# Optimization experiments

Hardware: AMD Instinct MI355X
Metric: run time of the kernel (lower is better)

## Reference

```python
import jax, jax.numpy as jnp
import numpy as np

N = 20000      # total atoms
M = 12         # neighbors per atom
B = 41         # nbr_fea_len
ORIG = 92      # orig_atom_fea_len
F = 64         # atom_fea_len
D = 2 * F + B  # 169, gated feature width
NC = 3         # n_conv
K = 3          # k parallel gates per conv
H = 128        # h_fea_len
N0 = 400       # crystals in batch
EPS = 1e-5     # batchnorm eps


def setup_inputs() -> dict:
    key = jax.random.key(0)
    ks = jax.random.split(key, 24)
    inp = {}
    inp["atom_fea"] = jax.random.normal(ks[0], (N, ORIG), jnp.float32)
    inp["nbr_fea"] = jax.random.normal(ks[1], (N, M, B), jnp.float32)
    inp["nbr_fea_idx"] = jax.random.randint(ks[2], (N, M), 0, N)
    inp["crystal_atom_idx"] = jnp.sort(jax.random.randint(ks[3], (N,), 0, N0))
    inp["n_crystals"] = N0
    inp["emb_w"] = jax.random.normal(ks[4], (ORIG, F)) * 0.1
    inp["emb_b"] = jnp.zeros((F,), jnp.float32)
    inp["fc_w"] = jax.random.normal(ks[5], (NC, K, D, D)) * 0.05
    inp["fc_b"] = jnp.zeros((NC, K, D), jnp.float32)
    inp["bn1_g"] = jnp.ones((NC, K, D), jnp.float32)
    inp["bn1_b"] = jnp.zeros((NC, K, D), jnp.float32)
    inp["bn1_m"] = jax.random.normal(ks[6], (NC, K, D)) * 0.1
    inp["bn1_v"] = jax.random.uniform(ks[7], (NC, K, D)) * 0.5 + 0.75
    inp["bn2_g"] = jnp.ones((NC, K, F), jnp.float32)
    inp["bn2_b"] = jnp.zeros((NC, K, F), jnp.float32)
    inp["bn2_m"] = jax.random.normal(ks[8], (NC, K, F)) * 0.1
    inp["bn2_v"] = jax.random.uniform(ks[9], (NC, K, F)) * 0.5 + 0.75
    inp["atom_w"] = jax.random.normal(ks[10], (NC, K, 2 * K)) * 0.3
    inp["atom_b"] = jnp.zeros((NC, 2 * K), jnp.float32)
    inp["nbr_w"] = jax.random.normal(ks[11], (NC, K, 2 * K)) * 0.3
    inp["nbr_b"] = jnp.zeros((NC, 2 * K), jnp.float32)
    inp["fc1_w"] = jax.random.normal(ks[12], (F, H)) * 0.1
    inp["fc1_b"] = jnp.zeros((H,), jnp.float32)
    inp["out_w"] = jax.random.normal(ks[13], (H, 1)) * 0.1
    inp["out_b"] = jnp.zeros((1,), jnp.float32)
    return inp


def _conv(atom_in, nbr, idx, fc_w, fc_b, bn1_g, bn1_b, bn1_m, bn1_v,
          bn2_g, bn2_b, bn2_m, bn2_v, atom_w, atom_b, nbr_w, nbr_b):
    n, m = idx.shape
    gathered = atom_in[idx]                                   # (N,M,F) irregular gather
    self_f = jnp.broadcast_to(atom_in[:, None, :], (n, m, F))
    total = jnp.concatenate([self_f, gathered, nbr], axis=2)  # (N,M,D)
    # k parallel linear layers, vectorized over k
    g = jnp.einsum('nmd,kde->knme', total, fc_w) + fc_b[:, None, None, :]  # (K,N,M,D)
    # bn1 (eval mode, running stats)
    g = (g - bn1_m[:, None, None, :]) * jax.lax.rsqrt(bn1_v[:, None, None, :] + EPS) \
        * bn1_g[:, None, None, :] + bn1_b[:, None, None, :]
    nbr_filter = jax.nn.softmax(g[..., :F], axis=2)            # softmax over neighbors M
    nbr_core = jax.nn.relu(g[..., F:2 * F])
    new_nbr_k = g[..., 2 * F:] + nbr[None]                     # (K,N,M,B) residual on bonds
    summed = jnp.sum(nbr_filter * nbr_core, axis=2)            # (K,N,F)
    summed = (summed - bn2_m[:, None, :]) * jax.lax.rsqrt(bn2_v[:, None, :] + EPS) \
        * bn2_g[:, None, :] + bn2_b[:, None, :]
    out_k = atom_in[None] + summed                             # (K,N,F) residual on atoms
    out = jnp.moveaxis(out_k, 0, 2)                            # (N,F,K)
    new_nbr = jnp.moveaxis(new_nbr_k, 0, 3)                    # (N,M,B,K)
    og = out @ atom_w + atom_b                                 # (N,F,2K)
    ng = new_nbr @ nbr_w + nbr_b                               # (N,M,B,2K)
    out = jnp.sum(og[..., :K] * jax.nn.softmax(og[..., K:], axis=2), axis=2)
    new_nbr = jnp.sum(ng[..., :K] * jax.nn.softmax(ng[..., K:], axis=3), axis=3)
    return out, new_nbr


def reference(atom_fea, nbr_fea, nbr_fea_idx, crystal_atom_idx, n_crystals,
              emb_w, emb_b, fc_w, fc_b, bn1_g, bn1_b, bn1_m, bn1_v,
              bn2_g, bn2_b, bn2_m, bn2_v, atom_w, atom_b, nbr_w, nbr_b,
              fc1_w, fc1_b, out_w, out_b):
    x = atom_fea @ emb_w + emb_b                               # embedding
    nbr = nbr_fea
    for i in range(NC):                                        # fixed small layer loop
        x, nbr = _conv(x, nbr, nbr_fea_idx,
                       fc_w[i], fc_b[i], bn1_g[i], bn1_b[i], bn1_m[i], bn1_v[i],
                       bn2_g[i], bn2_b[i], bn2_m[i], bn2_v[i],
                       atom_w[i], atom_b[i], nbr_w[i], nbr_b[i])
    # per-crystal mean pooling via segment sum
    sums = jax.ops.segment_sum(x, crystal_atom_idx, num_segments=n_crystals)
    counts = jax.ops.segment_sum(jnp.ones((x.shape[0], 1), x.dtype),
                                 crystal_atom_idx, num_segments=n_crystals)
    crys = sums / jnp.maximum(counts, 1.0)
    crys = jax.nn.relu(crys) @ fc1_w + fc1_b
    crys = jax.nn.relu(crys)
    return crys @ out_w + out_b                                # (N0, 1)
```

## Files before the change

kernel.cpp:

```cpp
#include <hip/hip_runtime.h>
#include <math.h>

#define N_ATOMS 20000
#define M 12
#define B 41
#define ORIG 92
#define F 64
#define D 169
#define NCONV 3
#define K 3
#define TWOK 6
#define H 128
#define N0 400
#define EPS 1e-5f
#define KB (K * B)
#define NBRS 42

#define KPAD 192
#define NS 6
#define ATOMS_PER_BLK 4
#define ROWS (ATOMS_PER_BLK * 16)
#define THREADS 512
#define LFRAG 98304
#define WT_USHORTS (NCONV * 2 * LFRAG)
#define GRID (N_ATOMS / ATOMS_PER_BLK)

typedef __attribute__((ext_vector_type(8))) short bf16x8;
typedef __attribute__((ext_vector_type(4))) float f32x4;

__device__ inline unsigned short f32_to_bf16(float v) {
    unsigned int x = __float_as_uint(v);
    unsigned int r = (x + 0x7fffu + ((x >> 16) & 1u)) >> 16;
    return (unsigned short)r;
}
__device__ inline float bf16_to_f32(unsigned short u) {
    return __uint_as_float(((unsigned int)u) << 16);
}
__device__ inline unsigned int pack_hilo(float v) {
    unsigned short hi = f32_to_bf16(v);
    unsigned short lo = f32_to_bf16(v - bf16_to_f32(hi));
    return (unsigned int)hi | ((unsigned int)lo << 16);
}
__device__ inline float unpack_hilo(unsigned int p) {
    return bf16_to_f32((unsigned short)(p & 0xFFFFu)) +
           bf16_to_f32((unsigned short)(p >> 16));
}

__global__ void emb_kernel(const float* __restrict__ atom_fea,
                           const float* __restrict__ emb_w,
                           const float* __restrict__ emb_b,
                           float* __restrict__ x,
                           unsigned int* __restrict__ xp) {
    int i = blockIdx.x * blockDim.x + threadIdx.x;
    if (i >= N_ATOMS * F) return;
    int n = i / F, f = i % F;
    const float* a = atom_fea + n * ORIG;
    float acc = emb_b[f];
    #pragma unroll 4
    for (int d = 0; d < ORIG; ++d)
        acc = fmaf(a[d], emb_w[d * F + f], acc);
    x[i] = acc;
    xp[i] = pack_hilo(acc);
}

__global__ void npack_kernel(const float* __restrict__ nbr_fea,
                             unsigned int* __restrict__ nbrp) {
    int i = blockIdx.x * blockDim.x + threadIdx.x;
    if (i >= N_ATOMS * M * NBRS) return;
    int nm = i / NBRS, slot = i - nm * NBRS;
    nbrp[i] = (slot < B) ? pack_hilo(nbr_fea[nm * B + slot]) : 0u;
}

__global__ void prep_kernel(const float* __restrict__ fc_w,
                            unsigned short* __restrict__ wt) {
    int i = blockIdx.x * blockDim.x + threadIdx.x;
    if (i >= NCONV * LFRAG) return;
    int layer = i / LFRAG;
    int r = i % LFRAG;
    int s = r / 16384;
    int r2 = r % 16384;
    int c16 = r2 / 512;
    int r3 = r2 % 512;
    int lane = r3 / 8;
    int e = r3 % 8;
    int col = c16 * 16 + (lane & 15);
    int k = s * 32 + (lane >> 4) * 8 + e;
    float v = 0.f;
    if (k < D) {
        int b3 = col >> 7, cc = col & 127;
        if (b3 < 3) {
            v = fc_w[((size_t)(layer * K + b3) * D + k) * D + cc];
        } else if (cc < KB) {
            int kk = cc / B, bb = cc - kk * B;
            v = fc_w[((size_t)(layer * K + kk) * D + k) * D + 2 * F + bb];
        }
    }
    unsigned short hi = f32_to_bf16(v);
    float hf = bf16_to_f32(hi);
    unsigned short lo = f32_to_bf16(v - hf);
    size_t off = (size_t)s * 16384 + c16 * 512 + lane * 8 + e;
    wt[(size_t)(layer * 2 + 0) * LFRAG + off] = hi;
    wt[(size_t)(layer * 2 + 1) * LFRAG + off] = lo;
}

__global__ void prep2_kernel(const float* __restrict__ fc_b,
                             const float* __restrict__ bn1_g,
                             const float* __restrict__ bn1_b,
                             const float* __restrict__ bn1_m,
                             const float* __restrict__ bn1_v,
                             const float* __restrict__ bn2_g,
                             const float* __restrict__ bn2_b,
                             const float* __restrict__ bn2_m,
                             const float* __restrict__ bn2_v,
                             float* __restrict__ sc1,
                             float* __restrict__ sh1,
                             float* __restrict__ sc2,
                             float* __restrict__ sh2) {
    int i = blockIdx.x * blockDim.x + threadIdx.x;
    if (i < NCONV * K * D) {
        float sc = bn1_g[i] * rsqrtf(bn1_v[i] + EPS);
        sc1[i] = sc;
        sh1[i] = fmaf(fc_b[i], sc, bn1_b[i] - bn1_m[i] * sc);
    }
    if (i < NCONV * K * F) {
        float sc = bn2_g[i] * rsqrtf(bn2_v[i] + EPS);
        sc2[i] = sc;
        sh2[i] = bn2_b[i] - bn2_m[i] * sc;
    }
}

template <bool NEED_NBR>
__global__ __launch_bounds__(THREADS, 4)
void conv_mfma(const float* __restrict__ xin,
               const unsigned int* __restrict__ xpin,
               const unsigned int* __restrict__ nbrpin,
               const int* __restrict__ idx,
               const unsigned short* __restrict__ wtl,
               const float* __restrict__ sc1,
               const float* __restrict__ sh1,
               const float* __restrict__ sc2,
               const float* __restrict__ sh2,
               const float* __restrict__ atom_w,
               const float* __restrict__ atom_b,
               const float* __restrict__ nbr_w,
               const float* __restrict__ nbr_b,
               float* __restrict__ xout,
               unsigned int* __restrict__ xpout,
               unsigned int* __restrict__ nbrpout) {
    __shared__ unsigned short s_a[2 * ROWS * KPAD];
    __shared__ float s_sum[ATOMS_PER_BLK * K * F];

    const int t = threadIdx.x;
    const int w = t >> 6;
    const int l = t & 63;
    const int l15 = l & 15;
    const int lane3 = l >> 4;
    const int n0 = blockIdx.x * ATOMS_PER_BLK;

    {
        const int srow = t >> 3;
        const int j8 = t & 7;
        const int a = srow >> 4, m = srow & 15;
        const int n = n0 + a;
        const unsigned int mask = (unsigned int)((srow & 7) << 4);
        char* hi_base = (char*)s_a + srow * (KPAD * 2);
        char* lo_base = hi_base + 2 * ROWS * KPAD;
        if (m < M) {
            const unsigned int* xs = xpin + n * F;
            const unsigned int* xg = xpin + idx[n * M + m] * F;
            const unsigned int* nb = nbrpin + (size_t)(n * M + m) * NBRS;
            #pragma unroll
            for (int q = 0; q < 12; ++q) {
                int kp = j8 + 8 * q;
                uint2 u;
                if (kp < 32)       u = *(const uint2*)&xs[kp * 2];
                else if (kp < 64)  u = *(const uint2*)&xg[kp * 2 - 64];
                else if (kp < 85)  u = *(const uint2*)&nb[kp * 2 - 128];
                else               u = make_uint2(0u, 0u);
                unsigned int hip = (u.x & 0xFFFFu) | (u.y << 16);
                unsigned int lop = (u.x >> 16) | (u.y & 0xFFFF0000u);
                unsigned int byo = ((unsigned int)(kp * 4)) ^ mask;
                *(unsigned int*)(hi_base + byo) = hip;
                *(unsigned int*)(lo_base + byo) = lop;
            }
        } else {
            #pragma unroll
            for (int q = 0; q < 12; ++q) {
                unsigned int byo = ((unsigned int)((j8 + 8 * q) * 4)) ^ mask;
                *(unsigned int*)(hi_base + byo) = 0u;
                *(unsigned int*)(lo_base + byo) = 0u;
            }
        }
    }
    __syncthreads();

    const int kk_gate = w >> 1, half = w & 1;
    int tile[4];
    if (w < 6) {
        tile[0] = kk_gate * 8 + half * 2 + 0;
        tile[1] = kk_gate * 8 + half * 2 + 1;
        tile[2] = tile[0] + 4;
        tile[3] = tile[1] + 4;
    } else {
        tile[0] = 24 + (w - 6) * 4 + 0;
        tile[1] = 24 + (w - 6) * 4 + 1;
        tile[2] = 24 + (w - 6) * 4 + 2;
        tile[3] = 24 + (w - 6) * 4 + 3;
    }

    f32x4 acc[ATOMS_PER_BLK][4];
    #pragma unroll
    for (int a = 0; a < ATOMS_PER_BLK; ++a)
        #pragma unroll
        for (int j = 0; j < 4; ++j)
            acc[a][j] = (f32x4){0.f, 0.f, 0.f, 0.f};

    if (!(w >= 6 && !NEED_NBR)) {
        for (int s = 0; s < NS; ++s) {
            bf16x8 ah[ATOMS_PER_BLK], al[ATOMS_PER_BLK];
            #pragma unroll
            for (int a = 0; a < ATOMS_PER_BLK; ++a) {
                int row = a * 16 + l15;
                int koff = s * 64 + lane3 * 16;
                int byte = row * (KPAD * 2) + (koff ^ ((row & 7) << 4));
                ah[a] = *reinterpret_cast<const bf16x8*>(&s_a[byte >> 1]);
                al[a] = *reinterpret_cast<const bf16x8*>(&s_a[(byte >> 1) + ROWS * KPAD]);
            }
            #pragma unroll
            for (int j = 0; j < 4; ++j) {
                const unsigned short* wp =
                    wtl + (size_t)s * 16384 + tile[j] * 512 + l * 8;
                bf16x8 bh = *reinterpret_cast<const bf16x8*>(wp);
                bf16x8 bl = *reinterpret_cast<const bf16x8*>(wp + LFRAG);
                #pragma unroll
                for (int a = 0; a < ATOMS_PER_BLK; ++a) {
                    acc[a][j] = __builtin_amdgcn_mfma_f32_16x16x32_bf16(ah[a], bh, acc[a][j], 0, 0, 0);
                    acc[a][j] = __builtin_amdgcn_mfma_f32_16x16x32_bf16(ah[a], bl, acc[a][j], 0, 0, 0);
                    acc[a][j] = __builtin_amdgcn_mfma_f32_16x16x32_bf16(al[a], bh, acc[a][j], 0, 0, 0);
                }
            }
        }
    }
    __syncthreads();

    float* s_nnk = reinterpret_cast<float*>(s_a);

    if (w < 6) {
        const int k = kk_gate;
        #pragma unroll
        for (int a = 0; a < ATOMS_PER_BLK; ++a) {
            #pragma unroll
            for (int j = 0; j < 2; ++j) {
                int e = (half * 2 + j) * 16 + l15;
                int cf = k * D + e, cr = cf + F, c2 = k * F + e;
                float sc_f = sc1[cf], sh_f = sh1[cf];
                float sc_c = sc1[cr], sh_c = sh1[cr];
                bool act = (lane3 < 3);
                float fv[4], cv[4];
                #pragma unroll
                for (int r = 0; r < 4; ++r) {
                    fv[r] = fmaf(acc[a][j][r], sc_f, sh_f);
                    cv[r] = fmaxf(fmaf(acc[a][j + 2][r], sc_c, sh_c), 0.f);
                }
                float mx = act ? fmaxf(fmaxf(fv[0], fv[1]), fmaxf(fv[2], fv[3])) : -1e30f;
                mx = fmaxf(mx, __shfl_xor(mx, 16));
                mx = fmaxf(mx, __shfl_xor(mx, 32));
                float se = 0.f, sp = 0.f;
                #pragma unroll
                for (int r = 0; r < 4; ++r) {
                    float ex = act ? __expf(fv[r] - mx) : 0.f;
                    se += ex;
                    sp = fmaf(ex, cv[r], sp);
                }
                se += __shfl_xor(se, 16);
                se += __shfl_xor(se, 32);
                sp += __shfl_xor(sp, 16);
                sp += __shfl_xor(sp, 32);
                float summed = sp / se;
                float outv = xin[(n0 + a) * F + e] + fmaf(summed, sc2[c2], sh2[c2]);
                if (lane3 == 0) s_sum[(a * K + k) * F + e] = outv;
            }
        }
    } else if (NEED_NBR) {
        #pragma unroll
        for (int a = 0; a < ATOMS_PER_BLK; ++a) {
            #pragma unroll
            for (int j = 0; j < 4; ++j) {
                int cc = (w - 6) * 64 + j * 16 + l15;
                if (cc < KB) {
                    int kk = cc / B, bb = cc - (cc / B) * B;
                    int col = kk * D + 2 * F + bb;
                    float sc = sc1[col], sh = sh1[col];
                    #pragma unroll
                    for (int r = 0; r < 4; ++r) {
                        int m = lane3 * 4 + r;
                        if (m < M) {
                            float nv = unpack_hilo(
                                nbrpin[(size_t)((n0 + a) * M + m) * NBRS + bb]);
                            s_nnk[((a * K + kk) * M + m) * B + bb] =
                                fmaf(acc[a][j][r], sc, sh) + nv;
                        }
                    }
                }
            }
        }
    }
    __syncthreads();

    if (t < ATOMS_PER_BLK * F) {
        int a2 = t >> 6, f = t & 63;
        float og[TWOK];
        #pragma unroll
        for (int j = 0; j < TWOK; ++j) {
            float v = atom_b[j];
            #pragma unroll
            for (int q = 0; q < K; ++q)
                v = fmaf(s_sum[(a2 * K + q) * F + f], atom_w[q * TWOK + j], v);
            og[j] = v;
        }
        float mx = fmaxf(fmaxf(og[K], og[K + 1]), og[K + 2]);
        float e0 = __expf(og[K] - mx), e1 = __expf(og[K + 1] - mx), e2 = __expf(og[K + 2] - mx);
        float inv = 1.f / (e0 + e1 + e2);
        float outv = (og[0] * e0 + og[1] * e1 + og[2] * e2) * inv;
        xout[(n0 + a2) * F + f] = outv;
        xpout[(n0 + a2) * F + f] = pack_hilo(outv);
    }

    if (NEED_NBR) {
        for (int i = t; i < ATOMS_PER_BLK * M * B; i += THREADS) {
            int a2 = i / (M * B);
            int r = i - a2 * (M * B);
            int m = r / B, b = r - m * B;
            float ng[TWOK];
            #pragma unroll
            for (int j = 0; j < TWOK; ++j) {
                float v = nbr_b[j];
                #pragma unroll
                for (int q = 0; q < K; ++q)
                    v = fmaf(s_nnk[((a2 * K + q) * M + m) * B + b], nbr_w[q * TWOK + j], v);
                ng[j] = v;
            }
            float mx = fmaxf(fmaxf(ng[K], ng[K + 1]), ng[K + 2]);
            float e0 = __expf(ng[K] - mx), e1 = __expf(ng[K + 1] - mx), e2 = __expf(ng[K + 2] - mx);
            float inv = 1.f / (e0 + e1 + e2);
            float v = (ng[0] * e0 + ng[1] * e1 + ng[2] * e2) * inv;
            nbrpout[(size_t)((n0 + a2) * M + m) * NBRS + b] = pack_hilo(v);
        }
        for (int i3 = t; i3 < ATOMS_PER_BLK * M; i3 += THREADS) {
            int a2 = i3 / M, m = i3 - a2 * M;
            nbrpout[(size_t)((n0 + a2) * M + m) * NBRS + B] = 0u;
        }
    }
}

__global__ void pool_kernel(const float* __restrict__ x,
                            const int* __restrict__ cidx,
                            float* __restrict__ sums,
                            float* __restrict__ cnt) {
    int i = blockIdx.x * blockDim.x + threadIdx.x;
    if (i >= N_ATOMS * F) return;
    int n = i / F, f = i % F;
    int c = cidx[n];
    atomicAdd(&sums[c * F + f], x[i]);
    if (f == 0) atomicAdd(&cnt[c], 1.0f);
}

__global__ void head_kernel(const float* __restrict__ sums,
                            const float* __restrict__ cnt,
                            const float* __restrict__ fc1_w,
                            const float* __restrict__ fc1_b,
                            const float* __restrict__ out_w,
                            const float* __restrict__ out_b,
                            float* __restrict__ out) {
    const int c = blockIdx.x;
    const int t = threadIdx.x;
    __shared__ float a[F];
    __shared__ float red[H];
    float inv_cnt = 1.f / fmaxf(cnt[c], 1.0f);
    if (t < F) a[t] = fmaxf(sums[c * F + t] * inv_cnt, 0.f);
    __syncthreads();
    float hv = fc1_b[t];
    #pragma unroll 4
    for (int f = 0; f < F; ++f)
        hv = fmaf(a[f], fc1_w[f * H + t], hv);
    hv = fmaxf(hv, 0.f);
    red[t] = hv * out_w[t];
    __syncthreads();
    for (int s = H / 2; s > 0; s >>= 1) {
        if (t < s) red[t] += red[t + s];
        __syncthreads();
    }
    if (t == 0) out[c] = red[0] + out_b[0];
}

extern "C" void kernel_launch(void* const* d_in, const int* in_sizes, int n_in,
                              void* d_out, int out_size, void* d_ws, size_t ws_size,
                              hipStream_t stream) {
    (void)in_sizes; (void)n_in; (void)out_size; (void)ws_size;
    const float* atom_fea = (const float*)d_in[0];
    const float* nbr_fea  = (const float*)d_in[1];
    const int*   nbr_idx  = (const int*)d_in[2];
    const int*   cidx     = (const int*)d_in[3];
    const float* emb_w = (const float*)d_in[5];
    const float* emb_b = (const float*)d_in[6];
    const float* fc_w  = (const float*)d_in[7];
    const float* fc_b  = (const float*)d_in[8];
    const float* bn1_g = (const float*)d_in[9];
    const float* bn1_b = (const float*)d_in[10];
    const float* bn1_m = (const float*)d_in[11];
    const float* bn1_v = (const float*)d_in[12];
    const float* bn2_g = (const float*)d_in[13];
    const float* bn2_b = (const float*)d_in[14];
    const float* bn2_m = (const float*)d_in[15];
    const float* bn2_v = (const float*)d_in[16];
    const float* atom_w = (const float*)d_in[17];
    const float* atom_b = (const float*)d_in[18];
    const float* nbr_w  = (const float*)d_in[19];
    const float* nbr_b  = (const float*)d_in[20];
    const float* fc1_w  = (const float*)d_in[21];
    const float* fc1_b  = (const float*)d_in[22];
    const float* out_w  = (const float*)d_in[23];
    const float* out_b  = (const float*)d_in[24];
    float* out = (float*)d_out;

    float* xA   = (float*)d_ws;
    float* xB   = xA + (size_t)N_ATOMS * F;
    unsigned int* xPA = (unsigned int*)(xB + (size_t)N_ATOMS * F);
    unsigned int* xPB = xPA + (size_t)N_ATOMS * F;
    unsigned int* nbrP0 = xPB + (size_t)N_ATOMS * F;
    unsigned int* nbrPA = nbrP0 + (size_t)N_ATOMS * M * NBRS;
    float* sums = (float*)(nbrPA + (size_t)N_ATOMS * M * NBRS);
    float* cnt  = sums + (size_t)N0 * F;
    float* sc1  = cnt + N0;
    float* sh1  = sc1 + NCONV * K * D;
    float* sc2  = sh1 + NCONV * K * D;
    float* sh2  = sc2 + NCONV * K * F;
    unsigned short* wt = (unsigned short*)(sh2 + NCONV * K * F);

    prep_kernel<<<(NCONV * LFRAG + 255) / 256, 256, 0, stream>>>(fc_w, wt);
    prep2_kernel<<<(NCONV * K * D + 255) / 256, 256, 0, stream>>>(
        fc_b, bn1_g, bn1_b, bn1_m, bn1_v, bn2_g, bn2_b, bn2_m, bn2_v,
        sc1, sh1, sc2, sh2);
    npack_kernel<<<(N_ATOMS * M * NBRS + 255) / 256, 256, 0, stream>>>(nbr_fea, nbrP0);
    emb_kernel<<<(N_ATOMS * F + 255) / 256, 256, 0, stream>>>(
        atom_fea, emb_w, emb_b, xA, xPA);

    conv_mfma<true><<<GRID, THREADS, 0, stream>>>(
        xA, xPA, nbrP0, nbr_idx,
        wt, sc1, sh1, sc2, sh2,
        atom_w, atom_b, nbr_w, nbr_b, xB, xPB, nbrPA);
    conv_mfma<true><<<GRID, THREADS, 0, stream>>>(
        xB, xPB, nbrPA, nbr_idx,
        wt + (size_t)2 * LFRAG,
        sc1 + (size_t)1 * K * D, sh1 + (size_t)1 * K * D,
        sc2 + (size_t)1 * K * F, sh2 + (size_t)1 * K * F,
        atom_w + (size_t)1 * K * TWOK, atom_b + (size_t)1 * TWOK,
        nbr_w + (size_t)1 * K * TWOK, nbr_b + (size_t)1 * TWOK, xA, xPA, nbrP0);
    conv_mfma<false><<<GRID, THREADS, 0, stream>>>(
        xA, xPA, nbrP0, nbr_idx,
        wt + (size_t)4 * LFRAG,
        sc1 + (size_t)2 * K * D, sh1 + (size_t)2 * K * D,
        sc2 + (size_t)2 * K * F, sh2 + (size_t)2 * K * F,
        atom_w + (size_t)2 * K * TWOK, atom_b + (size_t)2 * TWOK,
        nbr_w + (size_t)2 * K * TWOK, nbr_b + (size_t)2 * TWOK, xB, xPB, nbrPA);

    hipMemsetAsync(sums, 0, (size_t)(N0 * F + N0) * sizeof(float), stream);
    pool_kernel<<<(N_ATOMS * F + 255) / 256, 256, 0, stream>>>(xB, cidx, sums, cnt);
    head_kernel<<<N0, H, 0, stream>>>(sums, cnt, fc1_w, fc1_b, out_w, out_b, out);
}
```

Baseline: 617.4 us.

## Precompute per-atom self/neighbor projections once, shrink per-edge GEMM to bond features

The gated linear layer is split by input block. The self-atom and neighbor-atom parts of the weight matrix are applied once per atom in a new pq_kernel, which writes a wide per-atom P/Q buffer. The per-edge MFMA then covers only the 41 bond features (one 64-wide K slab instead of 192). The edge kernel adds P for its own atom and gathers Q rows for each neighbor before batch norm, and it updates the packed bond buffer in place instead of ping-ponging. This removes the repeated per-edge matmul over atom features, but it adds a large intermediate buffer write per layer and scattered scalar reads of Q from global memory.

```diff
diff --git a/kernel.cpp b/kernel.cpp
--- a/kernel.cpp
+++ b/kernel.cpp
@@ -16,13 +16,12 @@
 #define KB (K * B)
 #define NBRS 42
 
-#define KPAD 192
-#define NS 6
+#define PQW 1024
+#define LFRAG_PQ 65536
+#define LFRAG_BD 32768
 #define ATOMS_PER_BLK 4
-#define ROWS (ATOMS_PER_BLK * 16)
+#define ROWS 64
 #define THREADS 512
-#define LFRAG 98304
-#define WT_USHORTS (NCONV * 2 * LFRAG)
 #define GRID (N_ATOMS / ATOMS_PER_BLK)
 
 typedef __attribute__((ext_vector_type(8))) short bf16x8;
@@ -44,6 +43,17 @@
 __device__ inline float unpack_hilo(unsigned int p) {
     return bf16_to_f32((unsigned short)(p & 0xFFFFu)) +
            bf16_to_f32((unsigned short)(p >> 16));
+}
+
+__device__ inline float wlookup(const float* __restrict__ fc_w,
+                                int layer, int row, int c) {
+    int b3 = c >> 7, cc = c & 127;
+    if (b3 < 3) return fc_w[((size_t)(layer * K + b3) * D + row) * D + cc];
+    if (cc < KB) {
+        int kk = cc / B, bb = cc - kk * B;
+        return fc_w[((size_t)(layer * K + kk) * D + row) * D + 2 * F + bb];
+    }
+    return 0.f;
 }
 
 __global__ void emb_kernel(const float* __restrict__ atom_fea,
@@ -71,36 +81,45 @@
     nbrp[i] = (slot < B) ? pack_hilo(nbr_fea[nm * B + slot]) : 0u;
 }
 
-__global__ void prep_kernel(const float* __restrict__ fc_w,
-                            unsigned short* __restrict__ wt) {
+__global__ void prep_pq_kernel(const float* __restrict__ fc_w,
+                               unsigned short* __restrict__ wtpq) {
     int i = blockIdx.x * blockDim.x + threadIdx.x;
-    if (i >= NCONV * LFRAG) return;
-    int layer = i / LFRAG;
-    int r = i % LFRAG;
+    if (i >= NCONV * LFRAG_PQ) return;
+    int layer = i / LFRAG_PQ;
+    int r = i % LFRAG_PQ;
+    int s = r / 32768;
+    int r2 = r % 32768;
+    int c16 = r2 / 512;
+    int r3 = r2 % 512;
+    int lane = r3 / 8, e = r3 % 8;
+    int isQ = (c16 >= 32);
+    int c = (isQ ? c16 - 32 : c16) * 16 + (lane & 15);
+    int row = (isQ ? F : 0) + s * 32 + (lane >> 4) * 8 + e;
+    float v = wlookup(fc_w, layer, row, c);
+    unsigned short hi = f32_to_bf16(v);
+    unsigned short lo = f32_to_bf16(v - bf16_to_f32(hi));
+    wtpq[(size_t)(layer * 2 + 0) * LFRAG_PQ + r] = hi;
+    wtpq[(size_t)(layer * 2 + 1) * LFRAG_PQ + r] = lo;
+}
+
+__global__ void prep_bond_kernel(const float* __restrict__ fc_w,
+                                 unsigned short* __restrict__ wtb) {
+    int i = blockIdx.x * blockDim.x + threadIdx.x;
+    if (i >= NCONV * LFRAG_BD) return;
+    int layer = i / LFRAG_BD;
+    int r = i % LFRAG_BD;
     int s = r / 16384;
     int r2 = r % 16384;
     int c16 = r2 / 512;
     int r3 = r2 % 512;
-    int lane = r3 / 8;
-    int e = r3 % 8;
-    int col = c16 * 16 + (lane & 15);
-    int k = s * 32 + (lane >> 4) * 8 + e;
-    float v = 0.f;
-    if (k < D) {
-        int b3 = col >> 7, cc = col & 127;
-        if (b3 < 3) {
-            v = fc_w[((size_t)(layer * K + b3) * D + k) * D + cc];
-        } else if (cc < KB) {
-            int kk = cc / B, bb = cc - kk * B;
-            v = fc_w[((size_t)(layer * K + kk) * D + k) * D + 2 * F + bb];
-        }
-    }
+    int lane = r3 / 8, e = r3 % 8;
+    int c = c16 * 16 + (lane & 15);
+    int row = 2 * F + s * 32 + (lane >> 4) * 8 + e;
+    float v = (row < D) ? wlookup(fc_w, layer, row, c) : 0.f;
     unsigned short hi = f32_to_bf16(v);
-    float hf = bf16_to_f32(hi);
-    unsigned short lo = f32_to_bf16(v - hf);
-    size_t off = (size_t)s * 16384 + c16 * 512 + lane * 8 + e;
-    wt[(size_t)(layer * 2 + 0) * LFRAG + off] = hi;
-    wt[(size_t)(layer * 2 + 1) * LFRAG + off] = lo;
+    unsigned short lo = f32_to_bf16(v - bf16_to_f32(hi));
+    wtb[(size_t)(layer * 2 + 0) * LFRAG_BD + r] = hi;
+    wtb[(size_t)(layer * 2 + 1) * LFRAG_BD + r] = lo;
 }
 
 __global__ void prep2_kernel(const float* __restrict__ fc_b,
@@ -129,13 +148,85 @@
     }
 }
 
+__global__ __launch_bounds__(512, 4)
+void pq_kernel(const unsigned int* __restrict__ xp,
+               const unsigned short* __restrict__ wtl,
+               float* __restrict__ pq) {
+    __shared__ __align__(16) unsigned short s_a[2 * 32 * 64];
+
+    const int t = threadIdx.x;
+    const int w = t >> 6, l = t & 63;
+    const int l15 = l & 15, lane3 = l >> 4;
+    const int n0 = blockIdx.x * 32;
+
+    {
+        int row = t >> 4, j16 = t & 15;
+        unsigned int mask = (unsigned int)((row & 7) << 4);
+        char* hb = (char*)s_a + row * 128;
+        const unsigned int* xr = xp + (n0 + row) * F;
+        #pragma unroll
+        for (int q = 0; q < 2; ++q) {
+            int kp = j16 + 16 * q;
+            uint2 u = *(const uint2*)&xr[kp * 2];
+            unsigned int hip = (u.x & 0xFFFFu) | (u.y << 16);
+            unsigned int lop = (u.x >> 16) | (u.y & 0xFFFF0000u);
+            unsigned int byo = ((unsigned int)(kp * 4)) ^ mask;
+            *(unsigned int*)(hb + byo) = hip;
+            *(unsigned int*)(hb + byo + 4096) = lop;
+        }
+    }
+    __syncthreads();
+
+    f32x4 acc[2][8];
+    #pragma unroll
+    for (int a = 0; a < 2; ++a)
+        #pragma unroll
+        for (int tt = 0; tt < 8; ++tt)
+            acc[a][tt] = (f32x4){0.f, 0.f, 0.f, 0.f};
+
+    #pragma unroll
+    for (int s = 0; s < 2; ++s) {
+        bf16x8 ah[2], al[2];
+        #pragma unroll
+        for (int a = 0; a < 2; ++a) {
+            int row = a * 16 + l15;
+            int byte = row * 128 + ((s * 64 + lane3 * 16) ^ ((row & 7) << 4));
+            ah[a] = *(const bf16x8*)((const char*)s_a + byte);
+            al[a] = *(const bf16x8*)((const char*)s_a + byte + 4096);
+        }
+        #pragma unroll
+        for (int tt = 0; tt < 8; ++tt) {
+            const unsigned short* wp = wtl + s * 32768 + (w * 8 + tt) * 512 + l * 8;
+            bf16x8 bh = *(const bf16x8*)wp;
+            bf16x8 bl = *(const bf16x8*)(wp + LFRAG_PQ);
+            #pragma unroll
+            for (int a = 0; a < 2; ++a) {
+                acc[a][tt] = __builtin_amdgcn_mfma_f32_16x16x32_bf16(ah[a], bh, acc[a][tt], 0, 0, 0);
+                acc[a][tt] = __builtin_amdgcn_mfma_f32_16x16x32_bf16(ah[a], bl, acc[a][tt], 0, 0, 0);
+                acc[a][tt] = __builtin_amdgcn_mfma_f32_16x16x32_bf16(al[a], bh, acc[a][tt], 0, 0, 0);
+            }
+        }
+    }
+
+    #pragma unroll
+    for (int a = 0; a < 2; ++a)
+        #pragma unroll
+        for (int tt = 0; tt < 8; ++tt) {
+            int col = (w * 8 + tt) * 16 + l15;
+            int rowb = n0 + a * 16 + lane3 * 4;
+            #pragma unroll
+            for (int r = 0; r < 4; ++r)
+                pq[(size_t)(rowb + r) * PQW + col] = acc[a][tt][r];
+        }
+}
+
 template <bool NEED_NBR>
 __global__ __launch_bounds__(THREADS, 4)
 void conv_mfma(const float* __restrict__ xin,
-               const unsigned int* __restrict__ xpin,
-               const unsigned int* __restrict__ nbrpin,
+               unsigned int* __restrict__ nbrp,
                const int* __restrict__ idx,
                const unsigned short* __restrict__ wtl,
+               const float* __restrict__ pq,
                const float* __restrict__ sc1,
                const float* __restrict__ sh1,
                const float* __restrict__ sc2,
@@ -145,50 +236,42 @@
                const float* __restrict__ nbr_w,
                const float* __restrict__ nbr_b,
                float* __restrict__ xout,
-               unsigned int* __restrict__ xpout,
-               unsigned int* __restrict__ nbrpout) {
-    __shared__ unsigned short s_a[2 * ROWS * KPAD];
+               unsigned int* __restrict__ xpout) {
+    __shared__ __align__(16) char s_mem[24576];
     __shared__ float s_sum[ATOMS_PER_BLK * K * F];
+    __shared__ int s_idx[ATOMS_PER_BLK * M];
 
     const int t = threadIdx.x;
-    const int w = t >> 6;
-    const int l = t & 63;
-    const int l15 = l & 15;
-    const int lane3 = l >> 4;
+    const int w = t >> 6, l = t & 63;
+    const int l15 = l & 15, lane3 = l >> 4;
     const int n0 = blockIdx.x * ATOMS_PER_BLK;
 
+    if (t < ATOMS_PER_BLK * M) s_idx[t] = idx[n0 * M + t];
+
     {
-        const int srow = t >> 3;
-        const int j8 = t & 7;
-        const int a = srow >> 4, m = srow & 15;
-        const int n = n0 + a;
-        const unsigned int mask = (unsigned int)((srow & 7) << 4);
-        char* hi_base = (char*)s_a + srow * (KPAD * 2);
-        char* lo_base = hi_base + 2 * ROWS * KPAD;
+        int srow = t >> 3, j8 = t & 7;
+        int a = srow >> 4, m = srow & 15;
+        unsigned int mask = (unsigned int)((srow & 7) << 4);
+        char* hb = s_mem + srow * 128;
         if (m < M) {
-            const unsigned int* xs = xpin + n * F;
-            const unsigned int* xg = xpin + idx[n * M + m] * F;
-            const unsigned int* nb = nbrpin + (size_t)(n * M + m) * NBRS;
-            #pragma unroll
-            for (int q = 0; q < 12; ++q) {
+            const unsigned int* nb = nbrp + (size_t)((n0 + a) * M + m) * NBRS;
+            #pragma unroll
+            for (int q = 0; q < 4; ++q) {
                 int kp = j8 + 8 * q;
-                uint2 u;
-                if (kp < 32)       u = *(const uint2*)&xs[kp * 2];
-                else if (kp < 64)  u = *(const uint2*)&xg[kp * 2 - 64];
-                else if (kp < 85)  u = *(const uint2*)&nb[kp * 2 - 128];
-                else               u = make_uint2(0u, 0u);
+                uint2 u = (kp < 21) ? *(const uint2*)&nb[kp * 2]
+                                    : make_uint2(0u, 0u);
                 unsigned int hip = (u.x & 0xFFFFu) | (u.y << 16);
                 unsigned int lop = (u.x >> 16) | (u.y & 0xFFFF0000u);
                 unsigned int byo = ((unsigned int)(kp * 4)) ^ mask;
-                *(unsigned int*)(hi_base + byo) = hip;
-                *(unsigned int*)(lo_base + byo) = lop;
+                *(unsigned int*)(hb + byo) = hip;
+                *(unsigned int*)(hb + byo + 8192) = lop;
             }
         } else {
             #pragma unroll
-            for (int q = 0; q < 12; ++q) {
+            for (int q = 0; q < 4; ++q) {
                 unsigned int byo = ((unsigned int)((j8 + 8 * q) * 4)) ^ mask;
-                *(unsigned int*)(hi_base + byo) = 0u;
-                *(unsigned int*)(lo_base + byo) = 0u;
+                *(unsigned int*)(hb + byo) = 0u;
+                *(unsigned int*)(hb + byo + 8192) = 0u;
             }
         }
     }
@@ -216,22 +299,21 @@
             acc[a][j] = (f32x4){0.f, 0.f, 0.f, 0.f};
 
     if (!(w >= 6 && !NEED_NBR)) {
-        for (int s = 0; s < NS; ++s) {
+        #pragma unroll
+        for (int s = 0; s < 2; ++s) {
             bf16x8 ah[ATOMS_PER_BLK], al[ATOMS_PER_BLK];
             #pragma unroll
             for (int a = 0; a < ATOMS_PER_BLK; ++a) {
                 int row = a * 16 + l15;
-                int koff = s * 64 + lane3 * 16;
-                int byte = row * (KPAD * 2) + (koff ^ ((row & 7) << 4));
-                ah[a] = *reinterpret_cast<const bf16x8*>(&s_a[byte >> 1]);
-                al[a] = *reinterpret_cast<const bf16x8*>(&s_a[(byte >> 1) + ROWS * KPAD]);
+                int byte = row * 128 + ((s * 64 + lane3 * 16) ^ ((row & 7) << 4));
+                ah[a] = *(const bf16x8*)(s_mem + byte);
+                al[a] = *(const bf16x8*)(s_mem + byte + 8192);
             }
             #pragma unroll
             for (int j = 0; j < 4; ++j) {
-                const unsigned short* wp =
-                    wtl + (size_t)s * 16384 + tile[j] * 512 + l * 8;
-                bf16x8 bh = *reinterpret_cast<const bf16x8*>(wp);
-                bf16x8 bl = *reinterpret_cast<const bf16x8*>(wp + LFRAG);
+                const unsigned short* wp = wtl + s * 16384 + tile[j] * 512 + l * 8;
+                bf16x8 bh = *(const bf16x8*)wp;
+                bf16x8 bl = *(const bf16x8*)(wp + LFRAG_BD);
                 #pragma unroll
                 for (int a = 0; a < ATOMS_PER_BLK; ++a) {
                     acc[a][j] = __builtin_amdgcn_mfma_f32_16x16x32_bf16(ah[a], bh, acc[a][j], 0, 0, 0);
@@ -243,24 +325,32 @@
     }
     __syncthreads();
 
-    float* s_nnk = reinterpret_cast<float*>(s_a);
+    float* s_nnk = (float*)s_mem;
 
     if (w < 6) {
         const int k = kk_gate;
         #pragma unroll
         for (int a = 0; a < ATOMS_PER_BLK; ++a) {
-            #pragma unroll
-            for (int j = 0; j < 2; ++j) {
-                int e = (half * 2 + j) * 16 + l15;
+            const float* pqp = pq + (size_t)(n0 + a) * PQW;
+            #pragma unroll
+            for (int jp = 0; jp < 2; ++jp) {
+                int colf = tile[jp] * 16 + l15;
+                int colc = colf + 64;
+                int e = (half * 2 + jp) * 16 + l15;
                 int cf = k * D + e, cr = cf + F, c2 = k * F + e;
                 float sc_f = sc1[cf], sh_f = sh1[cf];
                 float sc_c = sc1[cr], sh_c = sh1[cr];
+                float Pf = pqp[colf], Pc = pqp[colc];
                 bool act = (lane3 < 3);
                 float fv[4], cv[4];
                 #pragma unroll
                 for (int r = 0; r < 4; ++r) {
-                    fv[r] = fmaf(acc[a][j][r], sc_f, sh_f);
-                    cv[r] = fmaxf(fmaf(acc[a][j + 2][r], sc_c, sh_c), 0.f);
+                    int mm = lane3 * 4 + r;
+                    int qn = s_idx[a * M + (mm < M ? mm : 0)];
+                    float Qf = pq[(size_t)qn * PQW + 512 + colf];
+                    float Qc = pq[(size_t)qn * PQW + 512 + colc];
+                    fv[r] = fmaf(acc[a][jp][r] + Pf + Qf, sc_f, sh_f);
+                    cv[r] = fmaxf(fmaf(acc[a][jp + 2][r] + Pc + Qc, sc_c, sh_c), 0.f);
                 }
                 float mx = act ? fmaxf(fmaxf(fv[0], fv[1]), fmaxf(fv[2], fv[3])) : -1e30f;
                 mx = fmaxf(mx, __shfl_xor(mx, 16));
@@ -284,21 +374,26 @@
     } else if (NEED_NBR) {
         #pragma unroll
         for (int a = 0; a < ATOMS_PER_BLK; ++a) {
+            const float* pqp = pq + (size_t)(n0 + a) * PQW;
             #pragma unroll
             for (int j = 0; j < 4; ++j) {
                 int cc = (w - 6) * 64 + j * 16 + l15;
                 if (cc < KB) {
-                    int kk = cc / B, bb = cc - (cc / B) * B;
-                    int col = kk * D + 2 * F + bb;
-                    float sc = sc1[col], sh = sh1[col];
+                    int kk = cc / B, bb = cc - kk * B;
+                    int col = 384 + cc;
+                    int scol = kk * D + 2 * F + bb;
+                    float sc = sc1[scol], sh = sh1[scol];
+                    float P1 = pqp[col];
                     #pragma unroll
                     for (int r = 0; r < 4; ++r) {
-                        int m = lane3 * 4 + r;
-                        if (m < M) {
+                        int mm = lane3 * 4 + r;
+                        if (mm < M) {
+                            int qn = s_idx[a * M + mm];
+                            float Q1 = pq[(size_t)qn * PQW + 512 + col];
                             float nv = unpack_hilo(
-                                nbrpin[(size_t)((n0 + a) * M + m) * NBRS + bb]);
-                            s_nnk[((a * K + kk) * M + m) * B + bb] =
-                                fmaf(acc[a][j][r], sc, sh) + nv;
+                                nbrp[(size_t)((n0 + a) * M + mm) * NBRS + bb]);
+                            s_nnk[((a * K + kk) * M + mm) * B + bb] =
+                                fmaf(acc[a][j][r] + P1 + Q1, sc, sh) + nv;
                         }
                     }
                 }
@@ -344,11 +439,7 @@
             float e0 = __expf(ng[K] - mx), e1 = __expf(ng[K + 1] - mx), e2 = __expf(ng[K + 2] - mx);
             float inv = 1.f / (e0 + e1 + e2);
             float v = (ng[0] * e0 + ng[1] * e1 + ng[2] * e2) * inv;
-            nbrpout[(size_t)((n0 + a2) * M + m) * NBRS + b] = pack_hilo(v);
-        }
-        for (int i3 = t; i3 < ATOMS_PER_BLK * M; i3 += THREADS) {
-            int a2 = i3 / M, m = i3 - a2 * M;
-            nbrpout[(size_t)((n0 + a2) * M + m) * NBRS + B] = 0u;
+            nbrp[(size_t)((n0 + a2) * M + m) * NBRS + b] = pack_hilo(v);
         }
     }
 }
@@ -427,42 +518,45 @@
     float* xB   = xA + (size_t)N_ATOMS * F;
     unsigned int* xPA = (unsigned int*)(xB + (size_t)N_ATOMS * F);
     unsigned int* xPB = xPA + (size_t)N_ATOMS * F;
-    unsigned int* nbrP0 = xPB + (size_t)N_ATOMS * F;
-    unsigned int* nbrPA = nbrP0 + (size_t)N_ATOMS * M * NBRS;
-    float* sums = (float*)(nbrPA + (size_t)N_ATOMS * M * NBRS);
+    unsigned int* nbrP = xPB + (size_t)N_ATOMS * F;
+    float* pqbuf = (float*)(nbrP + (size_t)N_ATOMS * M * NBRS);
+    float* sums = pqbuf + (size_t)N_ATOMS * PQW;
     float* cnt  = sums + (size_t)N0 * F;
     float* sc1  = cnt + N0;
     float* sh1  = sc1 + NCONV * K * D;
     float* sc2  = sh1 + NCONV * K * D;
     float* sh2  = sc2 + NCONV * K * F;
-    unsigned short* wt = (unsigned short*)(sh2 + NCONV * K * F);
-
-    prep_kernel<<<(NCONV * LFRAG + 255) / 256, 256, 0, stream>>>(fc_w, wt);
+    unsigned short* wtpq = (unsigned short*)(sh2 + NCONV * K * F);
+    unsigned short* wtb  = wtpq + (size_t)NCONV * 2 * LFRAG_PQ;
+
+    prep_pq_kernel<<<(NCONV * LFRAG_PQ + 255) / 256, 256, 0, stream>>>(fc_w, wtpq);
+    prep_bond_kernel<<<(NCONV * LFRAG_BD + 255) / 256, 256, 0, stream>>>(fc_w, wtb);
     prep2_kernel<<<(NCONV * K * D + 255) / 256, 256, 0, stream>>>(
         fc_b, bn1_g, bn1_b, bn1_m, bn1_v, bn2_g, bn2_b, bn2_m, bn2_v,
         sc1, sh1, sc2, sh2);
-    npack_kernel<<<(N_ATOMS * M * NBRS + 255) / 256, 256, 0, stream>>>(nbr_fea, nbrP0);
+    npack_kernel<<<(N_ATOMS * M * NBRS + 255) / 256, 256, 0, stream>>>(nbr_fea, nbrP);
     emb_kernel<<<(N_ATOMS * F + 255) / 256, 256, 0, stream>>>(
         atom_fea, emb_w, emb_b, xA, xPA);
 
+    pq_kernel<<<N_ATOMS / 32, 512, 0, stream>>>(xPA, wtpq, pqbuf);
     conv_mfma<true><<<GRID, THREADS, 0, stream>>>(
-        xA, xPA, nbrP0, nbr_idx,
-        wt, sc1, sh1, sc2, sh2,
-        atom_w, atom_b, nbr_w, nbr_b, xB, xPB, nbrPA);
+        xA, nbrP, nbr_idx, wtb, pqbuf,
+        sc1, sh1, sc2, sh2,
+        atom_w, atom_b, nbr_w, nbr_b, xB, xPB);
+    pq_kernel<<<N_ATOMS / 32, 512, 0, stream>>>(xPB, wtpq + (size_t)2 * LFRAG_PQ, pqbuf);
     conv_mfma<true><<<GRID, THREADS, 0, stream>>>(
-        xB, xPB, nbrPA, nbr_idx,
-        wt + (size_t)2 * LFRAG,
+        xB, nbrP, nbr_idx, wtb + (size_t)2 * LFRAG_BD, pqbuf,
         sc1 + (size_t)1 * K * D, sh1 + (size_t)1 * K * D,
         sc2 + (size_t)1 * K * F, sh2 + (size_t)1 * K * F,
         atom_w + (size_t)1 * K * TWOK, atom_b + (size_t)1 * TWOK,
-        nbr_w + (size_t)1 * K * TWOK, nbr_b + (size_t)1 * TWOK, xA, xPA, nbrP0);
+        nbr_w + (size_t)1 * K * TWOK, nbr_b + (size_t)1 * TWOK, xA, xPA);
+    pq_kernel<<<N_ATOMS / 32, 512, 0, stream>>>(xPA, wtpq + (size_t)4 * LFRAG_PQ, pqbuf);
     conv_mfma<false><<<GRID, THREADS, 0, stream>>>(
-        xA, xPA, nbrP0, nbr_idx,
-        wt + (size_t)4 * LFRAG,
+        xA, nbrP, nbr_idx, wtb + (size_t)4 * LFRAG_BD, pqbuf,
         sc1 + (size_t)2 * K * D, sh1 + (size_t)2 * K * D,
         sc2 + (size_t)2 * K * F, sh2 + (size_t)2 * K * F,
         atom_w + (size_t)2 * K * TWOK, atom_b + (size_t)2 * TWOK,
-        nbr_w + (size_t)2 * K * TWOK, nbr_b + (size_t)2 * TWOK, xB, xPB, nbrPA);
+        nbr_w + (size_t)2 * K * TWOK, nbr_b + (size_t)2 * TWOK, xB, xPB);
 
     hipMemsetAsync(sums, 0, (size_t)(N0 * F + N0) * sizeof(float), stream);
     pool_kernel<<<(N_ATOMS * F + 255) / 256, 256, 0, stream>>>(xB, cidx, sums, cnt);
```

Result: slower. 630.7 us (+2.2%).
